# Optimization experiments

Hardware: AMD Instinct MI355X
Metric: run time of the kernel (lower is better)

The kernel has to match this reference:

```python
import jax, jax.numpy as jnp
import numpy as np


def setup_inputs() -> dict:
    key = jax.random.key(0)
    ks = jax.random.split(key, 8)
    B, C, H, W = 4, 512, 64, 64
    C8 = C // 8
    return {
        "x": jax.random.normal(ks[0], (B, C, H, W), dtype=jnp.float32),
        "Wq": jax.random.normal(ks[1], (C8, C), dtype=jnp.float32) * 0.02,
        "bq": jax.random.normal(ks[2], (C8,), dtype=jnp.float32) * 0.02,
        "Wk": jax.random.normal(ks[3], (C8, C), dtype=jnp.float32) * 0.02,
        "bk": jax.random.normal(ks[4], (C8,), dtype=jnp.float32) * 0.02,
        "Wv": jax.random.normal(ks[5], (C, C), dtype=jnp.float32) * 0.02,
        "bv": jax.random.normal(ks[6], (C,), dtype=jnp.float32) * 0.02,
        "gamma": jax.random.normal(ks[7], (1,), dtype=jnp.float32),
    }


def reference(x, Wq, bq, Wk, bk, Wv, bv, gamma):
    B, C, H, W = x.shape
    N = H * W
    xf = x.reshape(B, C, N)  # 1x1 conv == per-position matmul over channels
    q = jnp.einsum('oc,bcn->bno', Wq, xf) + bq  # B, N, C//8  (proj_query^T)
    k = jnp.einsum('oc,bcn->bon', Wk, xf) + bk[None, :, None]  # B, C//8, N
    v = jnp.einsum('oc,bcn->bon', Wv, xf) + bv[None, :, None]  # B, C, N
    energy = jnp.einsum('bno,bom->bnm', q, k)  # B, N, N
    attention = jax.nn.softmax(energy, axis=-1)
    # out = bmm(proj_value, attention^T): out[:, :, n] = sum_m v[:, :, m] * att[n, m]
    out = jnp.einsum('bcm,bnm->bcn', v, attention).reshape(B, C, H, W)
    return gamma[0] * out + x
```

## Files before the change

### kernel.cpp

```cpp
#include <hip/hip_runtime.h>
#include <stdint.h>


typedef unsigned short u16;
typedef unsigned char u8;
typedef __attribute__((ext_vector_type(8))) short short8;
typedef __attribute__((ext_vector_type(4))) float f32x4;
typedef __attribute__((ext_vector_type(16))) float f32x16;
typedef __attribute__((ext_vector_type(4))) int i32x4;
typedef __attribute__((ext_vector_type(8))) int i32x8;

#define ASYNC16(gp, lp)                                                        \
  __builtin_amdgcn_global_load_lds(                                            \
      (__attribute__((address_space(1))) void*)(void*)(gp),                    \
      (__attribute__((address_space(3))) void*)(lp), 16, 0, 0)

#define WAIT_VM0 0x0F70
#define WAIT_VM6 0x0F76
#define WAIT_LGKM0 0xC07F

#define EXP_SHIFT 5.0f
#define EXP_CAP 57000.0f

__device__ __forceinline__ u16 f2bf(float f) {
  uint32_t u = __float_as_uint(f);
  u += 0x7FFFu + ((u >> 16) & 1u);
  return (u16)(u >> 16);
}

__device__ __forceinline__ u8 f2fp8(float f) {
  f = fminf(fmaxf(f, -440.f), 440.f);
  int r = __builtin_amdgcn_cvt_pk_fp8_f32(f, f, 0, false);
  return (u8)(r & 0xFF);
}

__global__ __launch_bounds__(256) void k_transpose(const float* __restrict__ x,
                                                   u16* __restrict__ xT) {
  __shared__ float tile[32][33];
  const int b = blockIdx.z;
  const int nb = blockIdx.x * 32;
  const int cb = blockIdx.y * 32;
  const int t = threadIdx.x;
  {
    const int nl = t & 31, c0 = t >> 5;
    const float* xp = x + ((size_t)b * 512 + cb) * 4096 + nb;
#pragma unroll
    for (int i = 0; i < 4; ++i) {
      const int cl = c0 + i * 8;
      tile[cl][nl] = xp[(size_t)cl * 4096 + nl];
    }
  }
  __syncthreads();
  {
    const int cl = t & 31, n0 = t >> 5;
    u16* xtp = xT + ((size_t)b * 4096 + nb) * 512 + cb;
#pragma unroll
    for (int i = 0; i < 4; ++i) {
      const int nl = n0 + i * 8;
      xtp[(size_t)nl * 512 + cl] = f2bf(tile[cl][nl]);
    }
  }
}

__global__ __launch_bounds__(256) void k_wcast(const float* __restrict__ Wq,
                                               const float* __restrict__ Wk,
                                               const float* __restrict__ Wv,
                                               u16* __restrict__ wqk,
                                               u16* __restrict__ wv) {
  const int idx = blockIdx.x * 256 + threadIdx.x;
  if (idx < 128 * 512) {
    const int r = idx >> 9, c = idx & 511;
    const float f = (r < 64) ? Wq[r * 512 + c] : Wk[(r - 64) * 512 + c];
    wqk[idx] = f2bf(f);
  } else {
    const int j = idx - 128 * 512;
    if (j < 512 * 512) wv[j] = f2bf(Wv[j]);
  }
}

__device__ __forceinline__ void gemm_bt_tile(const u16* __restrict__ A,
                                             const u16* __restrict__ B,
                                             const int K, const int rowA0,
                                             const int colB0, u16* smem,
                                             f32x4 acc[4][4]) {
  const int t = threadIdx.x;
  const int lane = t & 63, wave = t >> 6;
  const int quad = lane >> 4, l15 = lane & 15;
  const int wr = wave >> 1, wc = wave & 1;
  u16* As = smem;
  u16* Bs = smem + 8192;
  const f32x4 zero = {0.f, 0.f, 0.f, 0.f};
#pragma unroll
  for (int i = 0; i < 4; ++i)
#pragma unroll
    for (int j = 0; j < 4; ++j) acc[i][j] = zero;

  const int srow = t >> 3;
  const int c8 = (lane & 7) ^ (lane >> 3);
  const u16* ga = A + (size_t)(rowA0 + srow) * K + c8 * 8;
  const u16* gb = B + (size_t)(colB0 + srow) * K + c8 * 8;
  char* la = (char*)As + wave * 1024;
  char* lb = (char*)Bs + wave * 1024;
  const size_t rK32 = (size_t)32 * K;

  const int sw0 = (quad) ^ (l15 & 7);
  const int sw1 = (4 + quad) ^ (l15 & 7);

  for (int k0 = 0; k0 < K; k0 += 64) {
    ASYNC16(ga + k0, la);
    ASYNC16(ga + k0 + rK32, la + 4096);
    ASYNC16(ga + k0 + 2 * rK32, la + 8192);
    ASYNC16(ga + k0 + 3 * rK32, la + 12288);
    ASYNC16(gb + k0, lb);
    ASYNC16(gb + k0 + rK32, lb + 4096);
    ASYNC16(gb + k0 + 2 * rK32, lb + 8192);
    ASYNC16(gb + k0 + 3 * rK32, lb + 12288);
    __syncthreads();
#pragma unroll
    for (int s = 0; s < 2; ++s) {
      const int sw = s ? sw1 : sw0;
      short8 a[4], b[4];
#pragma unroll
      for (int i = 0; i < 4; ++i)
        a[i] = *(const short8*)(As + (wr * 64 + i * 16 + l15) * 64 + sw * 8);
#pragma unroll
      for (int j = 0; j < 4; ++j)
        b[j] = *(const short8*)(Bs + (wc * 64 + j * 16 + l15) * 64 + sw * 8);
#pragma unroll
      for (int i = 0; i < 4; ++i)
#pragma unroll
        for (int j = 0; j < 4; ++j)
          acc[i][j] = __builtin_amdgcn_mfma_f32_16x16x32_bf16(a[i], b[j],
                                                              acc[i][j], 0, 0, 0);
    }
    __syncthreads();
  }
}

__global__ __launch_bounds__(256) void k_proj_qk(const u16* __restrict__ xT,
                                                 const u16* __restrict__ wqk,
                                                 const float* __restrict__ bq,
                                                 const float* __restrict__ bk,
                                                 u16* __restrict__ q,
                                                 u16* __restrict__ kT) {
  __shared__ u16 smem[16384];
  const int b = blockIdx.z;
  const int rowA0 = blockIdx.x * 128;
  f32x4 acc[4][4];
  gemm_bt_tile(xT + (size_t)b * 4096 * 512, wqk, 512, rowA0, 0, smem, acc);
  const int t = threadIdx.x, lane = t & 63, wave = t >> 6;
  const int quad = lane >> 4, l15 = lane & 15;
  const int wr = wave >> 1, wc = wave & 1;
#pragma unroll
  for (int j = 0; j < 4; ++j) {
    const int col = wc * 64 + j * 16 + l15;
    const float bias = (col < 64) ? bq[col] : bk[col - 64];
#pragma unroll
    for (int i = 0; i < 4; ++i) {
#pragma unroll
      for (int r = 0; r < 4; ++r) {
        const int row = rowA0 + wr * 64 + i * 16 + quad * 4 + r;
        const float val = acc[i][j][r] + bias;
        if (col < 64)
          q[((size_t)b * 4096 + row) * 64 + col] = f2bf(val);
        else
          kT[((size_t)b * 4096 + row) * 64 + (col - 64)] = f2bf(val);
      }
    }
  }
}

__global__ __launch_bounds__(256) void k_proj_v(const u16* __restrict__ wv,
                                                const u16* __restrict__ xT,
                                                const float* __restrict__ bv,
                                                u8* __restrict__ v8) {
  __shared__ u16 smem[16384];
  const int b = blockIdx.z;
  const int rowA0 = blockIdx.x * 128;
  const int colB0 = blockIdx.y * 128;
  f32x4 acc[4][4];
  gemm_bt_tile(wv, xT + (size_t)b * 4096 * 512, 512, rowA0, colB0, smem, acc);
  const int t = threadIdx.x, lane = t & 63, wave = t >> 6;
  const int quad = lane >> 4, l15 = lane & 15;
  const int wr = wave >> 1, wc = wave & 1;
#pragma unroll
  for (int i = 0; i < 4; ++i) {
#pragma unroll
    for (int r = 0; r < 4; ++r) {
      const int row = rowA0 + wr * 64 + i * 16 + quad * 4 + r;
      const float bias = bv[row];
#pragma unroll
      for (int j = 0; j < 4; ++j) {
        const int col = colB0 + wc * 64 + j * 16 + l15;
        v8[((size_t)b * 512 + row) * 4096 + col] = f2fp8(acc[i][j][r] + bias);
      }
    }
  }
}

__global__ __launch_bounds__(512, 2) void k_fused(const u16* __restrict__ q,
                                                  const u16* __restrict__ kT,
                                                  const u8* __restrict__ v8,
                                                  const float* __restrict__ x,
                                                  const float* __restrict__ gamma,
                                                  float* __restrict__ out) {
  __shared__ u16 k_lds[2][128 * 64];
  __shared__ u8 v_lds[2][2][256 * 64];
  __shared__ u8 P_lds[2][128 * 64];
  __shared__ float lsum_lds[128];

  const int t = threadIdx.x;
  const int l = t & 63, w = t >> 6;
  const int quad = l >> 4, l15 = l & 15;
  const int l31 = l & 31, h = l >> 5;

  const int n0 = blockIdx.x * 128;
  const int c0 = blockIdx.y * 256;
  const int b = blockIdx.z;

  const u16* qg = q + ((size_t)b * 4096 + n0) * 64;
  const u16* kg = kT + (size_t)b * 4096 * 64;
  const u8* vg = v8 + ((size_t)b * 512 + c0) * 4096;

  const int p0 = t, p1 = t + 512;
  const int kr0 = p0 >> 3, kc0 = p0 & 7;
  const int kr1 = p1 >> 3, kc1 = p1 & 7;
  const u16* qs0 = qg + kr0 * 64 + (kc0 ^ (kr0 & 7)) * 8;
  const u16* qs1 = qg + kr1 * 64 + (kc1 ^ (kr1 & 7)) * 8;
  const u16* ks0g = kg + kr0 * 64 + (kc0 ^ (kr0 & 7)) * 8;
  const u16* ks1g = kg + kr1 * 64 + (kc1 ^ (kr1 & 7)) * 8;
  const int vr0 = p0 >> 2, va0 = p0 & 3;
  const int vr1 = p1 >> 2, va1 = p1 & 3;
  const u8* vs0 = vg + (size_t)vr0 * 4096 + (va0 ^ ((vr0 >> 1) & 3)) * 16;
  const u8* vs1 = vg + (size_t)vr1 * 4096 + (va1 ^ ((vr1 >> 1) & 3)) * 16;

#define STAGE_F(bi, m0)                                                        \
  do {                                                                         \
    ASYNC16(ks0g + (m0) * 64, (char*)k_lds[bi] + w * 1024);                    \
    ASYNC16(ks1g + (m0) * 64, (char*)k_lds[bi] + 8192 + w * 1024);             \
    ASYNC16(vs0 + (m0), (char*)v_lds[bi][0] + w * 1024);                       \
    ASYNC16(vs1 + (m0), (char*)v_lds[bi][0] + 8192 + w * 1024);                \
    ASYNC16(vs0 + (m0) + 64, (char*)v_lds[bi][1] + w * 1024);                  \
    ASYNC16(vs1 + (m0) + 64, (char*)v_lds[bi][1] + 8192 + w * 1024);           \
  } while (0)

  ASYNC16(qs0, (char*)P_lds[0] + w * 1024);
  ASYNC16(qs1, (char*)P_lds[0] + 8192 + w * 1024);
  STAGE_F(0, 0);
  __builtin_amdgcn_s_waitcnt(WAIT_VM6);
  __builtin_amdgcn_s_barrier();
  asm volatile("" ::: "memory");
  const int sw0 = quad ^ (l15 & 7);
  const int sw1 = (4 + quad) ^ (l15 & 7);
  const u16* qrow = (const u16*)P_lds[0] + (w * 16 + l15) * 64;
  const short8 af0 = *(const short8*)(qrow + sw0 * 8);
  const short8 af1 = *(const short8*)(qrow + sw1 * 8);
  asm volatile("" ::: "memory");
  __builtin_amdgcn_s_waitcnt(WAIT_LGKM0);
  __builtin_amdgcn_s_barrier();
  asm volatile("" ::: "memory");

  const int wrp = w >> 2, wcp = w & 3;
  int rowA[4], sA1[4], sA2[4];
#pragma unroll
  for (int i = 0; i < 4; ++i) {
    rowA[i] = wrp * 128 + i * 32 + l31;
    const int fa = (rowA[i] >> 1) & 3;
    sA1[i] = (2 * h) ^ fa;
    sA2[i] = (2 * h + 1) ^ fa;
  }
  const int rowB = wcp * 32 + l31;
  const int fbB = (rowB >> 1) & 3;
  const int sB1 = (2 * h) ^ fbB;
  const int sB2 = (2 * h + 1) ^ fbB;

  const int fbW = (l15 >> 1) & 3;
  u8* Pw = P_lds[0] + ((w * 16 + l15) * 64) + quad * 4;

  f32x16 acc[4];
#pragma unroll
  for (int i = 0; i < 4; ++i)
#pragma unroll
    for (int r = 0; r < 16; ++r) acc[i][r] = 0.f;

  float lsum = 0.f;
  const f32x4 zero = {0.f, 0.f, 0.f, 0.f};

  for (int it = 0; it < 32; ++it) {
    __builtin_amdgcn_s_waitcnt(WAIT_VM0);
    asm volatile("" ::: "memory");
    __builtin_amdgcn_s_barrier();
    asm volatile("" ::: "memory");
    const int cur = it & 1;
    if (it + 1 < 32) STAGE_F(cur ^ 1, (it + 1) * 128);

    const u16* kb = k_lds[cur];
    f32x4 eacc[8];
#pragma unroll
    for (int j = 0; j < 8; ++j) eacc[j] = zero;
    __builtin_amdgcn_s_setprio(1);
#pragma unroll
    for (int j = 0; j < 8; ++j)
      eacc[j] = __builtin_amdgcn_mfma_f32_16x16x32_bf16(
          *(const short8*)(kb + (j * 16 + l15) * 64 + sw0 * 8), af0, eacc[j],
          0, 0, 0);
#pragma unroll
    for (int j = 0; j < 8; ++j)
      eacc[j] = __builtin_amdgcn_mfma_f32_16x16x32_bf16(
          *(const short8*)(kb + (j * 16 + l15) * 64 + sw1 * 8), af1, eacc[j],
          0, 0, 0);
    __builtin_amdgcn_s_setprio(0);

#pragma unroll
    for (int j = 0; j < 8; ++j) {
      const float e0 = fminf(__expf(eacc[j][0] - EXP_SHIFT), EXP_CAP);
      const float e1 = fminf(__expf(eacc[j][1] - EXP_SHIFT), EXP_CAP);
      const float e2 = fminf(__expf(eacc[j][2] - EXP_SHIFT), EXP_CAP);
      const float e3 = fminf(__expf(eacc[j][3] - EXP_SHIFT), EXP_CAP);
      lsum += (e0 + e1) + (e2 + e3);
      int pk = __builtin_amdgcn_cvt_pk_bf8_f32(e0, e1, 0, false);
      pk = __builtin_amdgcn_cvt_pk_bf8_f32(e2, e3, pk, true);
      *(int*)(Pw + (j >> 2) * 8192 + ((j & 3) ^ fbW) * 16) = pk;
    }
    asm volatile("" ::: "memory");
    __builtin_amdgcn_s_waitcnt(WAIT_LGKM0);
    __builtin_amdgcn_s_barrier();
    asm volatile("" ::: "memory");

#pragma unroll
    for (int ks = 0; ks < 2; ++ks) {
      const u8* Vb = v_lds[cur][ks];
      const u8* Pb = P_lds[ks];
      i32x8 bb;
      {
        const u8* pb = Pb + rowB * 64;
        const i32x4 blo = *(const i32x4*)(pb + sB1 * 16);
        const i32x4 bhi = *(const i32x4*)(pb + sB2 * 16);
        bb[0] = blo[0]; bb[1] = blo[1]; bb[2] = blo[2]; bb[3] = blo[3];
        bb[4] = bhi[0]; bb[5] = bhi[1]; bb[6] = bhi[2]; bb[7] = bhi[3];
      }
      __builtin_amdgcn_s_setprio(1);
#pragma unroll
      for (int i = 0; i < 4; ++i) {
        const u8* pa = Vb + rowA[i] * 64;
        const i32x4 lo = *(const i32x4*)(pa + sA1[i] * 16);
        const i32x4 hi = *(const i32x4*)(pa + sA2[i] * 16);
        i32x8 a;
        a[0] = lo[0]; a[1] = lo[1]; a[2] = lo[2]; a[3] = lo[3];
        a[4] = hi[0]; a[5] = hi[1]; a[6] = hi[2]; a[7] = hi[3];
        acc[i] = __builtin_amdgcn_mfma_scale_f32_32x32x64_f8f6f4(
            a, bb, acc[i], 0 , 1 , 0, 0x7F, 0, 0x7F);
      }
      __builtin_amdgcn_s_setprio(0);
    }
    asm volatile("" ::: "memory");
  }
#undef STAGE_F

  lsum += __shfl_xor(lsum, 16);
  lsum += __shfl_xor(lsum, 32);
  if (l < 16) lsum_lds[w * 16 + l15] = lsum;
  asm volatile("" ::: "memory");
  __builtin_amdgcn_s_waitcnt(WAIT_LGKM0);
  __builtin_amdgcn_s_barrier();
  asm volatile("" ::: "memory");

  const float g = gamma[0];
  const int col = n0 + wcp * 32 + l31;
  const float gil = g / lsum_lds[wcp * 32 + l31];
#pragma unroll
  for (int i = 0; i < 4; ++i) {
#pragma unroll
    for (int r = 0; r < 16; ++r) {
      const int rloc = (r & 3) + 8 * (r >> 2) + 4 * h;
      const int row = c0 + wrp * 128 + i * 32 + rloc;
      const size_t idx = ((size_t)b * 512 + row) * 4096 + col;
      out[idx] = gil * acc[i][r] + x[idx];
    }
  }
}

extern "C" void kernel_launch(void* const* d_in, const int* in_sizes, int n_in,
                              void* d_out, int out_size, void* d_ws,
                              size_t ws_size, hipStream_t stream) {
  const float* x = (const float*)d_in[0];
  const float* Wq = (const float*)d_in[1];
  const float* bq = (const float*)d_in[2];
  const float* Wk = (const float*)d_in[3];
  const float* bk = (const float*)d_in[4];
  const float* Wv = (const float*)d_in[5];
  const float* bv = (const float*)d_in[6];
  const float* gamma = (const float*)d_in[7];
  float* out = (float*)d_out;

  char* ws = (char*)d_ws;
  u16* xT = (u16*)(ws);
  u16* wqk = (u16*)(ws + 16777216);
  u16* wv = (u16*)(ws + 16908288);
  u16* qb = (u16*)(ws + 17432576);
  u16* ktb = (u16*)(ws + 19529728);
  u8* v8 = (u8*)(ws + 21626880);

  k_transpose<<<dim3(128, 16, 4), 256, 0, stream>>>(x, xT);
  k_wcast<<<dim3(1280), 256, 0, stream>>>(Wq, Wk, Wv, wqk, wv);
  k_proj_qk<<<dim3(32, 1, 4), 256, 0, stream>>>(xT, wqk, bq, bk, qb, ktb);
  k_proj_v<<<dim3(4, 32, 4), 256, 0, stream>>>(wv, xT, bv, v8);
  k_fused<<<dim3(32, 2, 4), 512, 0, stream>>>(qb, ktb, v8, x, gamma, out);
}
```

Baseline: 207.2 us.

## Split fused attention across 16 waves and merge Q/K and V projection launches

The fused attention kernel now runs with 1024 threads per block. Waves are split into two halves over the key dimension of each 128-key tile, and each wave holds half as many output-channel accumulators. Partial softmax row sums from both halves are combined through LDS before normalisation. The Q/K projection and V projection kernels are merged into one launch that branches on blockIdx.y. The aim is more waves per CU to hide latency and one fewer kernel launch. The cost is fewer registers per thread, with the launch bounds hint (1024, 4) possibly forcing register pressure or spills.

Measured after the change: 196.1 us. 1.06x faster.

```diff
diff --git a/kernel.cpp b/kernel.cpp
--- a/kernel.cpp
+++ b/kernel.cpp
@@ -16,7 +16,9 @@
       (__attribute__((address_space(3))) void*)(lp), 16, 0, 0)
 
 #define WAIT_VM0 0x0F70
-#define WAIT_VM6 0x0F76
+#define WAIT_VM3 0x0F73
+#define WAIT_VM4 0x0F74
+#define WAIT_VM8 0x0F78
 #define WAIT_LGKM0 0xC07F
 
 #define EXP_SHIFT 5.0f
@@ -137,77 +139,71 @@
   }
 }
 
-__global__ __launch_bounds__(256) void k_proj_qk(const u16* __restrict__ xT,
-                                                 const u16* __restrict__ wqk,
-                                                 const float* __restrict__ bq,
-                                                 const float* __restrict__ bk,
-                                                 u16* __restrict__ q,
-                                                 u16* __restrict__ kT) {
+__global__ __launch_bounds__(256) void k_proj(const u16* __restrict__ xT,
+                                              const u16* __restrict__ wqk,
+                                              const u16* __restrict__ wv,
+                                              const float* __restrict__ bq,
+                                              const float* __restrict__ bk,
+                                              const float* __restrict__ bv,
+                                              u16* __restrict__ q,
+                                              u16* __restrict__ kT,
+                                              u8* __restrict__ v8) {
   __shared__ u16 smem[16384];
   const int b = blockIdx.z;
-  const int rowA0 = blockIdx.x * 128;
-  f32x4 acc[4][4];
-  gemm_bt_tile(xT + (size_t)b * 4096 * 512, wqk, 512, rowA0, 0, smem, acc);
+  const int by = blockIdx.y;
   const int t = threadIdx.x, lane = t & 63, wave = t >> 6;
   const int quad = lane >> 4, l15 = lane & 15;
   const int wr = wave >> 1, wc = wave & 1;
-#pragma unroll
-  for (int j = 0; j < 4; ++j) {
-    const int col = wc * 64 + j * 16 + l15;
-    const float bias = (col < 64) ? bq[col] : bk[col - 64];
+  f32x4 acc[4][4];
+
+  if (by == 4) {
+    const int rowA0 = blockIdx.x * 128;
+    gemm_bt_tile(xT + (size_t)b * 4096 * 512, wqk, 512, rowA0, 0, smem, acc);
+#pragma unroll
+    for (int j = 0; j < 4; ++j) {
+      const int col = wc * 64 + j * 16 + l15;
+      const float bias = (col < 64) ? bq[col] : bk[col - 64];
+#pragma unroll
+      for (int i = 0; i < 4; ++i) {
+#pragma unroll
+        for (int r = 0; r < 4; ++r) {
+          const int row = rowA0 + wr * 64 + i * 16 + quad * 4 + r;
+          const float val = acc[i][j][r] + bias;
+          if (col < 64)
+            q[((size_t)b * 4096 + row) * 64 + col] = f2bf(val);
+          else
+            kT[((size_t)b * 4096 + row) * 64 + (col - 64)] = f2bf(val);
+        }
+      }
+    }
+  } else {
+    const int rowA0 = by * 128;
+    const int colB0 = blockIdx.x * 128;
+    gemm_bt_tile(wv, xT + (size_t)b * 4096 * 512, 512, rowA0, colB0, smem, acc);
 #pragma unroll
     for (int i = 0; i < 4; ++i) {
 #pragma unroll
       for (int r = 0; r < 4; ++r) {
         const int row = rowA0 + wr * 64 + i * 16 + quad * 4 + r;
-        const float val = acc[i][j][r] + bias;
-        if (col < 64)
-          q[((size_t)b * 4096 + row) * 64 + col] = f2bf(val);
-        else
-          kT[((size_t)b * 4096 + row) * 64 + (col - 64)] = f2bf(val);
+        const float bias = bv[row];
+#pragma unroll
+        for (int j = 0; j < 4; ++j) {
+          const int col = colB0 + wc * 64 + j * 16 + l15;
+          v8[((size_t)b * 512 + row) * 4096 + col] = f2fp8(acc[i][j][r] + bias);
+        }
       }
     }
   }
 }
 
-__global__ __launch_bounds__(256) void k_proj_v(const u16* __restrict__ wv,
-                                                const u16* __restrict__ xT,
-                                                const float* __restrict__ bv,
-                                                u8* __restrict__ v8) {
-  __shared__ u16 smem[16384];
-  const int b = blockIdx.z;
-  const int rowA0 = blockIdx.x * 128;
-  const int colB0 = blockIdx.y * 128;
-  f32x4 acc[4][4];
-  gemm_bt_tile(wv, xT + (size_t)b * 4096 * 512, 512, rowA0, colB0, smem, acc);
-  const int t = threadIdx.x, lane = t & 63, wave = t >> 6;
-  const int quad = lane >> 4, l15 = lane & 15;
-  const int wr = wave >> 1, wc = wave & 1;
-#pragma unroll
-  for (int i = 0; i < 4; ++i) {
-#pragma unroll
-    for (int r = 0; r < 4; ++r) {
-      const int row = rowA0 + wr * 64 + i * 16 + quad * 4 + r;
-      const float bias = bv[row];
-#pragma unroll
-      for (int j = 0; j < 4; ++j) {
-        const int col = colB0 + wc * 64 + j * 16 + l15;
-        v8[((size_t)b * 512 + row) * 4096 + col] = f2fp8(acc[i][j][r] + bias);
-      }
-    }
-  }
-}
-
-__global__ __launch_bounds__(512, 2) void k_fused(const u16* __restrict__ q,
-                                                  const u16* __restrict__ kT,
-                                                  const u8* __restrict__ v8,
-                                                  const float* __restrict__ x,
-                                                  const float* __restrict__ gamma,
-                                                  float* __restrict__ out) {
+__global__ __launch_bounds__(1024, 4) void k_fused(
+    const u16* __restrict__ q, const u16* __restrict__ kT,
+    const u8* __restrict__ v8, const float* __restrict__ x,
+    const float* __restrict__ gamma, float* __restrict__ out) {
   __shared__ u16 k_lds[2][128 * 64];
   __shared__ u8 v_lds[2][2][256 * 64];
   __shared__ u8 P_lds[2][128 * 64];
-  __shared__ float lsum_lds[128];
+  __shared__ float lsum_lds[2][128];
 
   const int t = threadIdx.x;
   const int l = t & 63, w = t >> 6;
@@ -222,37 +218,28 @@
   const u16* kg = kT + (size_t)b * 4096 * 64;
   const u8* vg = v8 + ((size_t)b * 512 + c0) * 4096;
 
-  const int p0 = t, p1 = t + 512;
-  const int kr0 = p0 >> 3, kc0 = p0 & 7;
-  const int kr1 = p1 >> 3, kc1 = p1 & 7;
-  const u16* qs0 = qg + kr0 * 64 + (kc0 ^ (kr0 & 7)) * 8;
-  const u16* qs1 = qg + kr1 * 64 + (kc1 ^ (kr1 & 7)) * 8;
-  const u16* ks0g = kg + kr0 * 64 + (kc0 ^ (kr0 & 7)) * 8;
-  const u16* ks1g = kg + kr1 * 64 + (kc1 ^ (kr1 & 7)) * 8;
-  const int vr0 = p0 >> 2, va0 = p0 & 3;
-  const int vr1 = p1 >> 2, va1 = p1 & 3;
-  const u8* vs0 = vg + (size_t)vr0 * 4096 + (va0 ^ ((vr0 >> 1) & 3)) * 16;
-  const u8* vs1 = vg + (size_t)vr1 * 4096 + (va1 ^ ((vr1 >> 1) & 3)) * 16;
+  const int kr = t >> 3, kc = t & 7;
+  const u16* qsg = qg + kr * 64 + (kc ^ (kr & 7)) * 8;
+  const u16* ksg = kg + kr * 64 + (kc ^ (kr & 7)) * 8;
+  const int vr = t >> 2, va = t & 3;
+  const u8* vsg = vg + (size_t)vr * 4096 + (va ^ ((vr >> 1) & 3)) * 16;
 
 #define STAGE_F(bi, m0)                                                        \
   do {                                                                         \
-    ASYNC16(ks0g + (m0) * 64, (char*)k_lds[bi] + w * 1024);                    \
-    ASYNC16(ks1g + (m0) * 64, (char*)k_lds[bi] + 8192 + w * 1024);             \
-    ASYNC16(vs0 + (m0), (char*)v_lds[bi][0] + w * 1024);                       \
-    ASYNC16(vs1 + (m0), (char*)v_lds[bi][0] + 8192 + w * 1024);                \
-    ASYNC16(vs0 + (m0) + 64, (char*)v_lds[bi][1] + w * 1024);                  \
-    ASYNC16(vs1 + (m0) + 64, (char*)v_lds[bi][1] + 8192 + w * 1024);           \
+    ASYNC16(ksg + (size_t)(m0) * 64, (char*)k_lds[bi] + w * 1024);             \
+    ASYNC16(vsg + (m0), (char*)v_lds[bi][0] + w * 1024);                       \
+    ASYNC16(vsg + (m0) + 64, (char*)v_lds[bi][1] + w * 1024);                  \
   } while (0)
 
-  ASYNC16(qs0, (char*)P_lds[0] + w * 1024);
-  ASYNC16(qs1, (char*)P_lds[0] + 8192 + w * 1024);
+  ASYNC16(qsg, (char*)P_lds[0] + w * 1024);
   STAGE_F(0, 0);
-  __builtin_amdgcn_s_waitcnt(WAIT_VM6);
+  __builtin_amdgcn_s_waitcnt(WAIT_VM3);
   __builtin_amdgcn_s_barrier();
   asm volatile("" ::: "memory");
+  const int mh = w >> 3, ng = w & 7;
   const int sw0 = quad ^ (l15 & 7);
   const int sw1 = (4 + quad) ^ (l15 & 7);
-  const u16* qrow = (const u16*)P_lds[0] + (w * 16 + l15) * 64;
+  const u16* qrow = (const u16*)P_lds[0] + (ng * 16 + l15) * 64;
   const short8 af0 = *(const short8*)(qrow + sw0 * 8);
   const short8 af1 = *(const short8*)(qrow + sw1 * 8);
   asm volatile("" ::: "memory");
@@ -261,10 +248,10 @@
   asm volatile("" ::: "memory");
 
   const int wrp = w >> 2, wcp = w & 3;
-  int rowA[4], sA1[4], sA2[4];
-#pragma unroll
-  for (int i = 0; i < 4; ++i) {
-    rowA[i] = wrp * 128 + i * 32 + l31;
+  int rowA[2], sA1[2], sA2[2];
+#pragma unroll
+  for (int i = 0; i < 2; ++i) {
+    rowA[i] = wrp * 64 + i * 32 + l31;
     const int fa = (rowA[i] >> 1) & 3;
     sA1[i] = (2 * h) ^ fa;
     sA2[i] = (2 * h + 1) ^ fa;
@@ -275,11 +262,11 @@
   const int sB2 = (2 * h + 1) ^ fbB;
 
   const int fbW = (l15 >> 1) & 3;
-  u8* Pw = P_lds[0] + ((w * 16 + l15) * 64) + quad * 4;
-
-  f32x16 acc[4];
-#pragma unroll
-  for (int i = 0; i < 4; ++i)
+  u8* Pw = P_lds[mh] + (ng * 16 + l15) * 64 + quad * 4;
+
+  f32x16 acc[2];
+#pragma unroll
+  for (int i = 0; i < 2; ++i)
 #pragma unroll
     for (int r = 0; r < 16; ++r) acc[i][r] = 0.f;
 
@@ -294,25 +281,25 @@
     const int cur = it & 1;
     if (it + 1 < 32) STAGE_F(cur ^ 1, (it + 1) * 128);
 
-    const u16* kb = k_lds[cur];
-    f32x4 eacc[8];
-#pragma unroll
-    for (int j = 0; j < 8; ++j) eacc[j] = zero;
+    const u16* kb = k_lds[cur] + mh * 64 * 64;
+    f32x4 eacc[4];
+#pragma unroll
+    for (int j = 0; j < 4; ++j) eacc[j] = zero;
     __builtin_amdgcn_s_setprio(1);
 #pragma unroll
-    for (int j = 0; j < 8; ++j)
+    for (int j = 0; j < 4; ++j)
       eacc[j] = __builtin_amdgcn_mfma_f32_16x16x32_bf16(
           *(const short8*)(kb + (j * 16 + l15) * 64 + sw0 * 8), af0, eacc[j],
           0, 0, 0);
 #pragma unroll
-    for (int j = 0; j < 8; ++j)
+    for (int j = 0; j < 4; ++j)
       eacc[j] = __builtin_amdgcn_mfma_f32_16x16x32_bf16(
           *(const short8*)(kb + (j * 16 + l15) * 64 + sw1 * 8), af1, eacc[j],
           0, 0, 0);
     __builtin_amdgcn_s_setprio(0);
 
 #pragma unroll
-    for (int j = 0; j < 8; ++j) {
+    for (int j = 0; j < 4; ++j) {
       const float e0 = fminf(__expf(eacc[j][0] - EXP_SHIFT), EXP_CAP);
       const float e1 = fminf(__expf(eacc[j][1] - EXP_SHIFT), EXP_CAP);
       const float e2 = fminf(__expf(eacc[j][2] - EXP_SHIFT), EXP_CAP);
@@ -320,7 +307,7 @@
       lsum += (e0 + e1) + (e2 + e3);
       int pk = __builtin_amdgcn_cvt_pk_bf8_f32(e0, e1, 0, false);
       pk = __builtin_amdgcn_cvt_pk_bf8_f32(e2, e3, pk, true);
-      *(int*)(Pw + (j >> 2) * 8192 + ((j & 3) ^ fbW) * 16) = pk;
+      *(int*)(Pw + ((j ^ fbW) * 16)) = pk;
     }
     asm volatile("" ::: "memory");
     __builtin_amdgcn_s_waitcnt(WAIT_LGKM0);
@@ -341,7 +328,7 @@
       }
       __builtin_amdgcn_s_setprio(1);
 #pragma unroll
-      for (int i = 0; i < 4; ++i) {
+      for (int i = 0; i < 2; ++i) {
         const u8* pa = Vb + rowA[i] * 64;
         const i32x4 lo = *(const i32x4*)(pa + sA1[i] * 16);
         const i32x4 hi = *(const i32x4*)(pa + sA2[i] * 16);
@@ -359,7 +346,7 @@
 
   lsum += __shfl_xor(lsum, 16);
   lsum += __shfl_xor(lsum, 32);
-  if (l < 16) lsum_lds[w * 16 + l15] = lsum;
+  if (l < 16) lsum_lds[mh][ng * 16 + l] = lsum;
   asm volatile("" ::: "memory");
   __builtin_amdgcn_s_waitcnt(WAIT_LGKM0);
   __builtin_amdgcn_s_barrier();
@@ -367,13 +354,14 @@
 
   const float g = gamma[0];
   const int col = n0 + wcp * 32 + l31;
-  const float gil = g / lsum_lds[wcp * 32 + l31];
-#pragma unroll
-  for (int i = 0; i < 4; ++i) {
+  const int nc = wcp * 32 + l31;
+  const float gil = g / (lsum_lds[0][nc] + lsum_lds[1][nc]);
+#pragma unroll
+  for (int i = 0; i < 2; ++i) {
 #pragma unroll
     for (int r = 0; r < 16; ++r) {
       const int rloc = (r & 3) + 8 * (r >> 2) + 4 * h;
-      const int row = c0 + wrp * 128 + i * 32 + rloc;
+      const int row = c0 + wrp * 64 + i * 32 + rloc;
       const size_t idx = ((size_t)b * 512 + row) * 4096 + col;
       out[idx] = gil * acc[i][r] + x[idx];
     }
@@ -403,7 +391,7 @@
 
   k_transpose<<<dim3(128, 16, 4), 256, 0, stream>>>(x, xT);
   k_wcast<<<dim3(1280), 256, 0, stream>>>(Wq, Wk, Wv, wqk, wv);
-  k_proj_qk<<<dim3(32, 1, 4), 256, 0, stream>>>(xT, wqk, bq, bk, qb, ktb);
-  k_proj_v<<<dim3(4, 32, 4), 256, 0, stream>>>(wv, xT, bv, v8);
-  k_fused<<<dim3(32, 2, 4), 512, 0, stream>>>(qb, ktb, v8, x, gamma, out);
-}
+  k_proj<<<dim3(32, 5, 4), 256, 0, stream>>>(xT, wqk, wv, bq, bk, bv,
+                                             qb, ktb, v8);
+  k_fused<<<dim3(32, 2, 4), 1024, 0, stream>>>(qb, ktb, v8, x, gamma, out);
+}
```
